# Performance work log

Measured on AMD Instinct MI355X. Metric: run time of the kernel, lower is better.

The kernel has to match this reference:

```python
import jax, jax.numpy as jnp
import numpy as np

B, S, D, H = 16, 1024, 512, 8
SCALES = (5, 10, None)


def setup_inputs() -> dict:
    key = jax.random.key(0)
    ks = jax.random.split(key, 7)
    x = jax.random.normal(ks[0], (B, S, D), jnp.float32)
    Wqkv = jax.random.normal(ks[1], (3, 3 * D, D), jnp.float32) * 0.02
    bqkv = jax.random.normal(ks[2], (3, 3 * D), jnp.float32) * 0.02
    Wo = jax.random.normal(ks[3], (3, D, D), jnp.float32) * 0.02
    bo = jax.random.normal(ks[4], (3, D), jnp.float32) * 0.02
    Wf = jax.random.normal(ks[5], (D, 3 * D), jnp.float32) * 0.02
    bf = jax.random.normal(ks[6], (D,), jnp.float32) * 0.02
    return {"x": x, "Wqkv": Wqkv, "bqkv": bqkv, "Wo": Wo, "bo": bo, "Wf": Wf, "bf": bf}


def _window_bias(seq_len, scale):
    # query j attends key k iff 0 <= j - k < scale (causal local window)
    i = jnp.arange(seq_len)
    d = i[:, None] - i[None, :]
    allowed = (d >= 0) & (d < scale)
    return jnp.where(allowed, 0.0, -jnp.inf).astype(jnp.float32)  # [S, S]


def _mha(x, Wqkv, bqkv, Wo, bo, bias):
    # x: [B, S, D]; packed in_proj like nn.MultiheadAttention
    b, s, d = x.shape
    hd = d // H
    qkv = x @ Wqkv.T + bqkv                      # [B, S, 3D]
    q, k, v = jnp.split(qkv, 3, axis=-1)
    q = q.reshape(b, s, H, hd) * (1.0 / np.sqrt(hd)).astype(x.dtype)
    k = k.reshape(b, s, H, hd)
    v = v.reshape(b, s, H, hd)
    scores = jnp.einsum("bqhd,bkhd->bhqk", q, k)  # [B, H, S, S]
    if bias is not None:
        scores = scores + bias                    # broadcast [S, S]
    p = jax.nn.softmax(scores, axis=-1)
    o = jnp.einsum("bhqk,bkhd->bqhd", p, v).reshape(b, s, d)
    return o @ Wo.T + bo


def reference(x, Wqkv, bqkv, Wo, bo, Wf, bf):
    s = x.shape[1]
    outs = []
    for i, scale in enumerate(SCALES):
        bias = None if scale is None else _window_bias(s, scale)
        outs.append(_mha(x, Wqkv[i], bqkv[i], Wo[i], bo[i], bias))
    combined = jnp.concatenate(outs, axis=-1)     # [B, S, 3D]
    return combined @ Wf.T + bf                   # [B, S, D]
```

## Files before the change

kernel.cpp:

```cpp
#include <hip/hip_runtime.h>
#include <hip/hip_bf16.h>
#include <hip/hip_fp16.h>


using f16 = _Float16;
typedef _Float16 f16x8 __attribute__((ext_vector_type(8)));
typedef _Float16 f16x2 __attribute__((ext_vector_type(2)));
typedef float    f32x4 __attribute__((ext_vector_type(4)));

__device__ inline void storeC(float* p, float v) { *p = v; }
__device__ inline void storeC(f16* p, float v)   { *p = (f16)v; }

__device__ inline void async_cp16(const f16* g, f16* l) {
    __builtin_amdgcn_global_load_lds(
        (const __attribute__((address_space(1))) unsigned int*)g,
        (__attribute__((address_space(3))) unsigned int*)l,
        16, 0, 0);
}

__global__ __launch_bounds__(256) void prep_all(
    const float* __restrict__ x, const float* __restrict__ Wqkv,
    const float* __restrict__ Wf, const float* __restrict__ Wo,
    const float* __restrict__ bo, const float* __restrict__ bfv,
    f16* __restrict__ xh, f16* __restrict__ wqkvh, f16* __restrict__ wfh,
    f16* __restrict__ WoT, float* __restrict__ bp)
{
    __shared__ float t[32][33];
    const int bid = blockIdx.x;
    const int tid = threadIdx.x;

    if (bid < 5632) {
        const float* in; f16* outp; int base;
        if (bid < 4096)      { in = x;    outp = xh;    base = bid; }
        else if (bid < 5248) { in = Wqkv; outp = wqkvh; base = bid - 4096; }
        else                 { in = Wf;   outp = wfh;   base = bid - 5248; }
        int i = (base * 256 + tid) * 8;
        float4 a = *(const float4*)(in + i);
        float4 b = *(const float4*)(in + i + 4);
        f16x8 h = { (f16)a.x, (f16)a.y, (f16)a.z, (f16)a.w,
                    (f16)b.x, (f16)b.y, (f16)b.z, (f16)b.w };
        *(f16x8*)(outp + i) = h;
    } else if (bid < 6400) {
        const int idx = bid - 5632;
        const int z  = idx >> 8;
        const int bx = (idx & 15) * 32;
        const int by = ((idx >> 4) & 15) * 32;
        const int tx = tid & 31;
        const int ty = tid >> 5;
#pragma unroll
        for (int r = ty; r < 32; r += 8)
            t[r][tx] = Wo[(size_t)z * 262144 + (by + r) * 512 + bx + tx];
        __syncthreads();
#pragma unroll
        for (int r = ty; r < 32; r += 8)
            WoT[(size_t)z * 262144 + (bx + r) * 512 + by + tx] = (f16)t[tx][r];
    } else {
        const int o = (bid - 6400) * 4 + (tid >> 6);
        const int lane = tid & 63;
        float s = 0.f;
        for (int j = lane; j < 1536; j += 64) s += Wf[o * 1536 + j] * bo[j];
#pragma unroll
        for (int msk = 1; msk < 64; msk <<= 1) s += __shfl_xor(s, msk, 64);
        if (lane == 0) bp[o] = s + bfv[o];
    }
}

template <typename TC>
__global__ __launch_bounds__(256) void gemm_mfma_nt(
    const f16* __restrict__ A, int lda, long azs,
    const f16* __restrict__ B, int ldb, long bzs,
    const float* __restrict__ bias,
    TC* __restrict__ C, int ldc, long czs,
    int K)
{
    __shared__ __align__(16) f16 As[2][128 * 32];
    __shared__ __align__(16) f16 Bs[2][128 * 32];

    const int tid  = threadIdx.x;
    const int lane = tid & 63;
    const int wave = tid >> 6;
    const int wm = (wave >> 1) * 64;
    const int wn = (wave & 1) * 64;
    const int bm = blockIdx.y * 128;
    const int bn = blockIdx.x * 128;
    const int z  = blockIdx.z;

    const int srow = tid >> 2;
    const int scol = (tid & 3) * 8;
    const int soff = srow * 32 + scol;

    const f16* Ag = A + (size_t)z * azs + (size_t)(bm + srow) * lda + scol;
    const f16* Bg = B + (size_t)z * bzs + (size_t)(bn + srow) * ldb + scol;

    f32x4 acc[4][4];
#pragma unroll
    for (int i = 0; i < 4; ++i)
#pragma unroll
        for (int j = 0; j < 4; ++j)
            acc[i][j] = (f32x4){0.f, 0.f, 0.f, 0.f};

    const int fr = lane & 15;
    const int fk = (lane >> 4) * 8;

    async_cp16(Ag, &As[0][soff]);
    async_cp16(Ag + (size_t)64 * lda, &As[0][soff + 64 * 32]);
    async_cp16(Bg, &Bs[0][soff]);
    async_cp16(Bg + (size_t)64 * ldb, &Bs[0][soff + 64 * 32]);

    const int nt = K >> 5;
    for (int t = 0; t < nt; ++t) {
        __syncthreads();
        const int p = t & 1;
        if (t + 1 < nt) {
            const int k1 = (t + 1) * 32;
            async_cp16(Ag + k1, &As[p ^ 1][soff]);
            async_cp16(Ag + k1 + (size_t)64 * lda, &As[p ^ 1][soff + 64 * 32]);
            async_cp16(Bg + k1, &Bs[p ^ 1][soff]);
            async_cp16(Bg + k1 + (size_t)64 * ldb, &Bs[p ^ 1][soff + 64 * 32]);
        }

        f16x8 af[4], bfr[4];
#pragma unroll
        for (int i = 0; i < 4; ++i)
            af[i] = *(const f16x8*)&As[p][(wm + i * 16 + fr) * 32 + fk];
#pragma unroll
        for (int j = 0; j < 4; ++j)
            bfr[j] = *(const f16x8*)&Bs[p][(wn + j * 16 + fr) * 32 + fk];
#pragma unroll
        for (int i = 0; i < 4; ++i)
#pragma unroll
            for (int j = 0; j < 4; ++j)
                acc[i][j] = __builtin_amdgcn_mfma_f32_16x16x32_f16(
                    af[i], bfr[j], acc[i][j], 0, 0, 0);
    }

    const int cn  = lane & 15;
    const int cr4 = (lane >> 4) * 4;
#pragma unroll
    for (int i = 0; i < 4; ++i) {
#pragma unroll
        for (int j = 0; j < 4; ++j) {
            const int col = bn + wn + j * 16 + cn;
            const float bv = bias ? bias[col] : 0.f;
#pragma unroll
            for (int r = 0; r < 4; ++r) {
                const int row = bm + wm + i * 16 + cr4 + r;
                storeC(&C[(size_t)z * czs + (size_t)row * ldc + col],
                       acc[i][j][r] + bv);
            }
        }
    }
}

template <int NR, typename TC>
__global__ __launch_bounds__(512, 2) void gemm_mfma_8ph(
    const f16* __restrict__ A, int lda,
    const f16* __restrict__ B, int ldb,
    const float* __restrict__ bias,
    TC* __restrict__ C, int ldc, int K)
{
    __shared__ __align__(16) f16 As[2][256 * 64];
    __shared__ __align__(16) f16 Bs[2][NR * 64 * 64];

    const int tid  = threadIdx.x;
    const int lane = tid & 63;
    const int wave = tid >> 6;
    const int wr = wave >> 2;
    const int wc = wave & 3;
    const int bm = blockIdx.y * 256;
    const int bn = blockIdx.x * (NR * 64);
    const int fr  = lane & 15;
    const int grp = lane >> 4;

    const int c0 = ((0 + grp) ^ (fr & 7)) * 8;
    const int c1 = ((4 + grp) ^ (fr & 7)) * 8;

    const int srow = tid >> 3;
    const int scol = ((tid & 7) ^ (srow & 7)) * 8;
    const f16* Ag = A + (size_t)(bm + srow) * lda + scol;
    const f16* Bg = B + (size_t)(bn + srow) * ldb + scol;

    f32x4 acc[8][NR];
#pragma unroll
    for (int m = 0; m < 8; ++m)
#pragma unroll
        for (int n = 0; n < NR; ++n)
            acc[m][n] = (f32x4){0.f, 0.f, 0.f, 0.f};

    const int arow = wr * 128 + fr;
    const int brow = wc * (NR * 16) + fr;

    f16x8 bfrag[NR][2];
    f16x8 aP[2][2], aQ[2][2];

    auto stage = [&](int p, int kt) {
        const f16* a_ = Ag + (size_t)kt * 64;
        const f16* b_ = Bg + (size_t)kt * 64;
        f16* al = &As[p][tid * 8];
        f16* bl = &Bs[p][tid * 8];
#pragma unroll
        for (int i = 0; i < 4; ++i)
            async_cp16(a_ + (size_t)(i * 64) * lda, al + i * 4096);
#pragma unroll
        for (int i = 0; i < NR; ++i)
            async_cp16(b_ + (size_t)(i * 64) * ldb, bl + i * 4096);
    };

    const int nt = K >> 6;

    stage(0, 0);
    stage(1, 1);

    for (int t = 0; t < nt; ++t) {
        const int p = t & 1;
        if (t + 1 < nt) {
            if constexpr (NR == 3)
                asm volatile("s_waitcnt vmcnt(7)" ::: "memory");
            else
                asm volatile("s_waitcnt vmcnt(6)" ::: "memory");
        } else {
            asm volatile("s_waitcnt vmcnt(0)" ::: "memory");
        }
        __builtin_amdgcn_s_barrier();

        const f16* asb = As[p];
        const f16* bsb = Bs[p];

        auto loada = [&](f16x8 (&d)[2][2], int mq) {
#pragma unroll
            for (int m2 = 0; m2 < 2; ++m2) {
                const int ro = (arow + (mq * 2 + m2) * 16) * 64;
                d[m2][0] = *(const f16x8*)&asb[ro + c0];
                d[m2][1] = *(const f16x8*)&asb[ro + c1];
            }
        };
        auto qmfma = [&](const f16x8 (&a_)[2][2], int mq) {
            __builtin_amdgcn_s_setprio(1);
#pragma unroll
            for (int m2 = 0; m2 < 2; ++m2)
#pragma unroll
                for (int n = 0; n < NR; ++n) {
                    f32x4 z = __builtin_amdgcn_mfma_f32_16x16x32_f16(
                        a_[m2][0], bfrag[n][0], acc[mq * 2 + m2][n], 0, 0, 0);
                    acc[mq * 2 + m2][n] = __builtin_amdgcn_mfma_f32_16x16x32_f16(
                        a_[m2][1], bfrag[n][1], z, 0, 0, 0);
                }
            __builtin_amdgcn_s_setprio(0);
        };

#pragma unroll
        for (int n = 0; n < NR; ++n) {
            const int ro = (brow + n * 16) * 64;
            bfrag[n][0] = *(const f16x8*)&bsb[ro + c0];
            bfrag[n][1] = *(const f16x8*)&bsb[ro + c1];
        }
        loada(aP, 0);
        asm volatile("s_waitcnt lgkmcnt(0)" ::: "memory");
        __builtin_amdgcn_sched_barrier(0);

        loada(aQ, 1);
        qmfma(aP, 0);
        asm volatile("s_waitcnt lgkmcnt(0)" ::: "memory");
        __builtin_amdgcn_sched_barrier(0);

        loada(aP, 2);
        qmfma(aQ, 1);
        asm volatile("s_waitcnt lgkmcnt(0)" ::: "memory");
        __builtin_amdgcn_sched_barrier(0);

        loada(aQ, 3);
        qmfma(aP, 2);
        asm volatile("s_waitcnt lgkmcnt(0)" ::: "memory");
        __builtin_amdgcn_sched_barrier(0);

        __builtin_amdgcn_s_barrier();
        if (t + 2 < nt) stage(p, t + 2);
        qmfma(aQ, 3);
    }

    const int cn  = lane & 15;
    const int cr4 = (lane >> 4) * 4;
#pragma unroll
    for (int m = 0; m < 8; ++m)
#pragma unroll
        for (int n = 0; n < NR; ++n) {
            const int col = bn + wc * (NR * 16) + n * 16 + cn;
            const float bv = bias ? bias[col] : 0.f;
#pragma unroll
            for (int r = 0; r < 4; ++r) {
                const int row = bm + wr * 128 + m * 16 + cr4 + r;
                storeC(&C[(size_t)row * ldc + col], acc[m][n][r] + bv);
            }
        }
}

__global__ __launch_bounds__(256) void win_attn_mfma(
    const f16* __restrict__ qkv, f16* __restrict__ out, int w)
{
    __shared__ __align__(16) f16 Vs[4][64 * 40];
    __shared__ __align__(16) f16 Ps[4][16 * 40];

    const int tid  = threadIdx.x;
    const int lane = tid & 63;
    const int wave = tid >> 6;
    const int b  = blockIdx.y;
    const int h  = blockIdx.z;
    const int q0 = (blockIdx.x * 4 + wave) * 16;
    const size_t bs = (size_t)b * 1024;

    const int fr  = lane & 15;
    const int grp = lane >> 4;
    const int fk8 = grp * 8;

    f16x8 aq[2];
    {
        const f16* qp = qkv + (bs + q0 + fr) * 1536 + h * 64 + fk8;
        aq[0] = *(const f16x8*)qp;
        aq[1] = *(const f16x8*)(qp + 32);
#pragma unroll
        for (int e = 0; e < 8; ++e) {
            aq[0][e] *= (f16)0.18033688;
            aq[1][e] *= (f16)0.18033688;
        }
    }

    f16x8 bk[2][2];
#pragma unroll
    for (int g = 0; g < 2; ++g) {
        int krow = q0 - 16 + g * 16 + fr;
        int kcl  = krow < 0 ? 0 : krow;
        const f16* kp = qkv + (bs + kcl) * 1536 + 512 + h * 64 + fk8;
        bk[g][0] = *(const f16x8*)kp;
        bk[g][1] = *(const f16x8*)(kp + 32);
    }

    {
        const int vk = lane & 31;
        const int vd = (lane >> 5) * 32;
        int vrow = q0 - 16 + vk;
        int vcl  = vrow < 0 ? 0 : vrow;
        const f16* vp = qkv + (bs + vcl) * 1536 + 1024 + h * 64 + vd;
        f16* vsw = Vs[wave];
#pragma unroll
        for (int t = 0; t < 4; ++t) {
            f16x8 vv = *(const f16x8*)(vp + t * 8);
#pragma unroll
            for (int e = 0; e < 8; ++e)
                vsw[(vd + t * 8 + e) * 40 + vk] = vv[e];
        }
    }

    f32x4 s[2];
#pragma unroll
    for (int g = 0; g < 2; ++g) {
        f32x4 z = (f32x4){0.f, 0.f, 0.f, 0.f};
        z = __builtin_amdgcn_mfma_f32_16x16x32_f16(aq[0], bk[g][0], z, 0, 0, 0);
        s[g] = __builtin_amdgcn_mfma_f32_16x16x32_f16(aq[1], bk[g][1], z, 0, 0, 0);
    }

    float l[4] = {0.f, 0.f, 0.f, 0.f};
#pragma unroll
    for (int g = 0; g < 2; ++g) {
        const int kpos = q0 - 16 + g * 16 + fr;
#pragma unroll
        for (int r = 0; r < 4; ++r) {
            const int diff = (grp * 4 + r) - (g * 16 + fr) + 16;
            const bool ok = (diff >= 0) && (diff < w) && (kpos >= 0);
            float p = ok ? exp2f(fminf(s[g][r], 15.9f)) : 0.f;
            l[r] += p;
            Ps[wave][(grp * 4 + r) * 40 + g * 16 + fr] = (f16)p;
        }
    }

    __builtin_amdgcn_wave_barrier();

    f16x8 pa = *(const f16x8*)&Ps[wave][fr * 40 + fk8];
    f32x4 acc[4];
#pragma unroll
    for (int j = 0; j < 4; ++j) {
        f16x8 bv = *(const f16x8*)&Vs[wave][(j * 16 + fr) * 40 + fk8];
        f32x4 z = (f32x4){0.f, 0.f, 0.f, 0.f};
        acc[j] = __builtin_amdgcn_mfma_f32_16x16x32_f16(pa, bv, z, 0, 0, 0);
    }

#pragma unroll
    for (int r = 0; r < 4; ++r)
#pragma unroll
        for (int msk = 1; msk < 16; msk <<= 1)
            l[r] += __shfl_xor(l[r], msk, 64);

#pragma unroll
    for (int j = 0; j < 4; ++j)
#pragma unroll
        for (int r = 0; r < 4; ++r) {
            const int q = q0 + grp * 4 + r;
            out[(bs + q) * 1536 + h * 64 + j * 16 + fr] = (f16)(acc[j][r] / l[r]);
        }
}

__global__ __launch_bounds__(256, 4) void full_attn_mfma(
    const f16* __restrict__ qkv, f16* __restrict__ out)
{
    __shared__ __align__(16) f16 Ks[2][64 * 72];
    __shared__ __align__(16) f16 Vs[2][64 * 72];

    const int tid  = threadIdx.x;
    const int lane = tid & 63;
    const int wave = tid >> 6;
    const int q0 = blockIdx.x * 128;
    const int b  = blockIdx.y;
    const int h  = blockIdx.z;
    const size_t bs = (size_t)b * 1024;

    const int fr  = lane & 15;
    const int grp = lane >> 4;
    const int fk8 = grp * 8;

    f16x8 aq[2][2];
#pragma unroll
    for (int qt = 0; qt < 2; ++qt) {
        const f16* qp = qkv + (bs + q0 + wave * 32 + qt * 16 + fr) * 1536
                        + h * 64 + fk8;
        aq[qt][0] = *(const f16x8*)qp;
        aq[qt][1] = *(const f16x8*)(qp + 32);
#pragma unroll
        for (int e = 0; e < 8; ++e) {
            aq[qt][0][e] *= (f16)0.18033688;
            aq[qt][1][e] *= (f16)0.18033688;
        }
    }

    f16x8 onesf;
#pragma unroll
    for (int e = 0; e < 8; ++e) onesf[e] = (f16)1.0f;

    const f32x4 fz = (f32x4){0.f, 0.f, 0.f, 0.f};
    f32x4 lacc[2] = {fz, fz};
    f32x4 acc[2][4];
#pragma unroll
    for (int qt = 0; qt < 2; ++qt)
#pragma unroll
        for (int j = 0; j < 4; ++j)
            acc[qt][j] = fz;

    const int kr = tid >> 2, kc = (tid & 3) * 16;
    const int kp = (tid & 31) * 2, cb = (tid >> 5) * 8;

    const f16* kgp = qkv + (bs + kr) * 1536 + 512 + h * 64 + kc;
    const f16* vgp = qkv + (bs + kp) * 1536 + 1024 + h * 64 + cb;

    f16x8 ka, kb, va, vb;
    ka = *(const f16x8*)kgp; kb = *(const f16x8*)(kgp + 8);
    va = *(const f16x8*)vgp; vb = *(const f16x8*)(vgp + 1536);

    {
        f16* ks = &Ks[0][kr * 72 + kc];
        *(f16x8*)ks = ka; *(f16x8*)(ks + 8) = kb;
        f16* vs = &Vs[0][kp];
#pragma unroll
        for (int e = 0; e < 8; ++e) {
            f16x2 pr = { va[e], vb[e] };
            *(f16x2*)&vs[(cb + e) * 72] = pr;
        }
    }
    kgp += 64 * 1536; vgp += 64 * 1536;
    ka = *(const f16x8*)kgp; kb = *(const f16x8*)(kgp + 8);
    va = *(const f16x8*)vgp; vb = *(const f16x8*)(vgp + 1536);

    for (int t = 0; t < 16; ++t) {
        __syncthreads();
        const int p = t & 1;

        if (t + 1 < 16) {
            f16* ks = &Ks[p ^ 1][kr * 72 + kc];
            *(f16x8*)ks = ka; *(f16x8*)(ks + 8) = kb;
            f16* vs = &Vs[p ^ 1][kp];
#pragma unroll
            for (int e = 0; e < 8; ++e) {
                f16x2 pr = { va[e], vb[e] };
                *(f16x2*)&vs[(cb + e) * 72] = pr;
            }
            if (t + 2 < 16) {
                kgp += 64 * 1536; vgp += 64 * 1536;
                ka = *(const f16x8*)kgp; kb = *(const f16x8*)(kgp + 8);
                va = *(const f16x8*)vgp; vb = *(const f16x8*)(vgp + 1536);
            }
        }

        f16x8 kf[4][2];
#pragma unroll
        for (int j = 0; j < 4; ++j)
#pragma unroll
            for (int c = 0; c < 2; ++c)
                kf[j][c] = *(const f16x8*)&Ks[p][(j * 16 + fr) * 72 + c * 32 + fk8];

        f16x8 paf[2][2];
#pragma unroll
        for (int qt = 0; qt < 2; ++qt) {
            f32x4 s2[4];
#pragma unroll
            for (int j = 0; j < 4; ++j) {
                f32x4 z = __builtin_amdgcn_mfma_f32_16x16x32_f16(
                        kf[j][0], aq[qt][0], fz, 0, 0, 0);
                s2[j] = __builtin_amdgcn_mfma_f32_16x16x32_f16(
                        kf[j][1], aq[qt][1], z, 0, 0, 0);
            }

            unsigned int dw[4][2];
#pragma unroll
            for (int j = 0; j < 4; ++j) {
                float p0 = exp2f(fminf(s2[j][0], 15.9f));
                float p1 = exp2f(fminf(s2[j][1], 15.9f));
                float p2 = exp2f(fminf(s2[j][2], 15.9f));
                float p3 = exp2f(fminf(s2[j][3], 15.9f));
                f16x2 h0 = { (f16)p0, (f16)p1 };
                f16x2 h1 = { (f16)p2, (f16)p3 };
                dw[j][0] = __builtin_bit_cast(unsigned int, h0);
                dw[j][1] = __builtin_bit_cast(unsigned int, h1);
            }

            unsigned int pdw[2][4];
#pragma unroll
            for (int c = 0; c < 2; ++c)
#pragma unroll
                for (int T = 0; T < 2; ++T) {
                    unsigned int X = dw[2 * c][T];
                    unsigned int Y = dw[2 * c + 1][T];
                    asm("v_permlane32_swap_b32 %0, %1" : "+v"(X), "+v"(Y));
                    asm("v_permlane16_swap_b32 %0, %1" : "+v"(X), "+v"(Y));
                    pdw[c][T]     = X;
                    pdw[c][2 + T] = Y;
                }
            union { unsigned int u[4]; f16x8 hv; } cu;
#pragma unroll
            for (int c = 0; c < 2; ++c) {
                cu.u[0] = pdw[c][0]; cu.u[1] = pdw[c][1];
                cu.u[2] = pdw[c][2]; cu.u[3] = pdw[c][3];
                paf[qt][c] = cu.hv;
            }

            lacc[qt] = __builtin_amdgcn_mfma_f32_16x16x32_f16(
                paf[qt][0], onesf, lacc[qt], 0, 0, 0);
            lacc[qt] = __builtin_amdgcn_mfma_f32_16x16x32_f16(
                paf[qt][1], onesf, lacc[qt], 0, 0, 0);
        }

        f16x8 vf[4][2];
#pragma unroll
        for (int j = 0; j < 4; ++j)
#pragma unroll
            for (int c = 0; c < 2; ++c)
                vf[j][c] = *(const f16x8*)&Vs[p][(j * 16 + fr) * 72 + c * 32 + fk8];

#pragma unroll
        for (int qt = 0; qt < 2; ++qt)
#pragma unroll
            for (int j = 0; j < 4; ++j)
#pragma unroll
                for (int c = 0; c < 2; ++c)
                    acc[qt][j] = __builtin_amdgcn_mfma_f32_16x16x32_f16(
                        paf[qt][c], vf[j][c], acc[qt][j], 0, 0, 0);
    }

#pragma unroll
    for (int qt = 0; qt < 2; ++qt) {
        float inv[4];
#pragma unroll
        for (int r = 0; r < 4; ++r) inv[r] = 1.0f / lacc[qt][r];
#pragma unroll
        for (int j = 0; j < 4; ++j)
#pragma unroll
            for (int r = 0; r < 4; ++r) {
                const int q = q0 + wave * 32 + qt * 16 + grp * 4 + r;
                out[(bs + q) * 1536 + h * 64 + j * 16 + fr] =
                    (f16)(acc[qt][j][r] * inv[r]);
            }
    }
}

extern "C" void kernel_launch(void* const* d_in, const int* in_sizes, int n_in,
                              void* d_out, int out_size, void* d_ws, size_t ws_size,
                              hipStream_t stream)
{
    const float* x    = (const float*)d_in[0];
    const float* Wqkv = (const float*)d_in[1];
    const float* bqkv = (const float*)d_in[2];
    const float* Wo   = (const float*)d_in[3];
    const float* bo   = (const float*)d_in[4];
    const float* Wf   = (const float*)d_in[5];
    const float* bfin = (const float*)d_in[6];
    float* out = (float*)d_out;

    char* ws = (char*)d_ws;
    f16*   qkvbuf   = (f16*)ws;
    f16*   attn_cat = (f16*)(ws + 50331648);
    f16*   wfh      = (f16*)(ws + 100663296);
    f16*   WoT      = (f16*)(ws + 102236160);
    f16*   Wfo      = (f16*)(ws + 103809024);
    float* bp       = (float*)(ws + 105381888);

    f16* xh    = (f16*)d_out;
    f16* wqkvh = (f16*)((char*)d_out + 16777216);

    prep_all<<<dim3(6528), 256, 0, stream>>>(
        x, Wqkv, Wf, Wo, bo, bfin, xh, wqkvh, wfh, WoT, bp);

    gemm_mfma_nt<f16><<<dim3(4, 4, 3), 256, 0, stream>>>(
        wfh, 1536, 512, WoT, 512, 262144, nullptr, Wfo, 1536, 512, 512);

    for (int i = 0; i < 3; ++i) {
        gemm_mfma_8ph<3, f16><<<dim3(8, 64), 512, 0, stream>>>(
            xh, 512, wqkvh + (size_t)i * 786432, 512, bqkv + i * 1536,
            qkvbuf, 1536, 512);

        if (i == 0)
            win_attn_mfma<<<dim3(16, 16, 8), 256, 0, stream>>>(
                qkvbuf, attn_cat + 0 * 512, 5);
        else if (i == 1)
            win_attn_mfma<<<dim3(16, 16, 8), 256, 0, stream>>>(
                qkvbuf, attn_cat + 1 * 512, 10);
        else
            full_attn_mfma<<<dim3(8, 16, 8), 256, 0, stream>>>(
                qkvbuf, attn_cat + 2 * 512);
    }

    gemm_mfma_8ph<2, float><<<dim3(4, 64), 512, 0, stream>>>(
        attn_cat, 1536, Wfo, 1536, bp, out, 512, 1536);
}
```

Baseline: 386.4 us.

## Batch the three QKV GEMMs and fuse all attention branches into one launch

The three per-scale QKV projections become a single batched GEMM launch using blockIdx.z strides, and each scale writes to its own QKV buffer. All three attention variants then run in one combined kernel that dispatches on block index, with the full-attention blocks scheduled first. The windowed attention body also keeps P in registers through permlane swaps and computes row sums with an MFMA against ones, instead of staging P in LDS and reducing with shuffles. The aim is fewer launches and tail gaps plus better occupancy overlap, at the cost of three times the QKV workspace, which is taken only if ws_size is large enough.

```diff
diff --git a/kernel.cpp b/kernel.cpp
--- a/kernel.cpp
+++ b/kernel.cpp
@@ -155,12 +155,17 @@
 template <int NR, typename TC>
 __global__ __launch_bounds__(512, 2) void gemm_mfma_8ph(
     const f16* __restrict__ A, int lda,
-    const f16* __restrict__ B, int ldb,
-    const float* __restrict__ bias,
-    TC* __restrict__ C, int ldc, int K)
+    const f16* __restrict__ B, int ldb, long bzs,
+    const float* __restrict__ bias, long bizs,
+    TC* __restrict__ C, int ldc, long czs, int K)
 {
     __shared__ __align__(16) f16 As[2][256 * 64];
     __shared__ __align__(16) f16 Bs[2][NR * 64 * 64];
+
+    const int z = blockIdx.z;
+    B += (size_t)z * bzs;
+    C += (size_t)z * czs;
+    const float* biasz = bias ? bias + (size_t)z * bizs : nullptr;
 
     const int tid  = threadIdx.x;
     const int lane = tid & 63;
@@ -207,7 +212,6 @@
     };
 
     const int nt = K >> 6;
-
     stage(0, 0);
     stage(1, 1);
 
@@ -240,10 +244,10 @@
             for (int m2 = 0; m2 < 2; ++m2)
 #pragma unroll
                 for (int n = 0; n < NR; ++n) {
-                    f32x4 z = __builtin_amdgcn_mfma_f32_16x16x32_f16(
+                    f32x4 zz = __builtin_amdgcn_mfma_f32_16x16x32_f16(
                         a_[m2][0], bfrag[n][0], acc[mq * 2 + m2][n], 0, 0, 0);
                     acc[mq * 2 + m2][n] = __builtin_amdgcn_mfma_f32_16x16x32_f16(
-                        a_[m2][1], bfrag[n][1], z, 0, 0, 0);
+                        a_[m2][1], bfrag[n][1], zz, 0, 0, 0);
                 }
             __builtin_amdgcn_s_setprio(0);
         };
@@ -285,7 +289,7 @@
 #pragma unroll
         for (int n = 0; n < NR; ++n) {
             const int col = bn + wc * (NR * 16) + n * 16 + cn;
-            const float bv = bias ? bias[col] : 0.f;
+            const float bv = biasz ? biasz[col] : 0.f;
 #pragma unroll
             for (int r = 0; r < 4; ++r) {
                 const int row = bm + wr * 128 + m * 16 + cr4 + r;
@@ -294,23 +298,21 @@
         }
 }
 
-__global__ __launch_bounds__(256) void win_attn_mfma(
-    const f16* __restrict__ qkv, f16* __restrict__ out, int w)
-{
-    __shared__ __align__(16) f16 Vs[4][64 * 40];
-    __shared__ __align__(16) f16 Ps[4][16 * 40];
-
+__device__ __forceinline__ void win_attn_body(
+    const f16* __restrict__ qkv, f16* __restrict__ out, f16* sm,
+    int w, int bx, int b, int h)
+{
     const int tid  = threadIdx.x;
     const int lane = tid & 63;
     const int wave = tid >> 6;
-    const int b  = blockIdx.y;
-    const int h  = blockIdx.z;
-    const int q0 = (blockIdx.x * 4 + wave) * 16;
+    const int q0 = (bx * 4 + wave) * 16;
     const size_t bs = (size_t)b * 1024;
 
     const int fr  = lane & 15;
     const int grp = lane >> 4;
     const int fk8 = grp * 8;
+
+    f16* vsw = sm + wave * 2560;
 
     f16x8 aq[2];
     {
@@ -340,7 +342,6 @@
         int vrow = q0 - 16 + vk;
         int vcl  = vrow < 0 ? 0 : vrow;
         const f16* vp = qkv + (bs + vcl) * 1536 + 1024 + h * 64 + vd;
-        f16* vsw = Vs[wave];
 #pragma unroll
         for (int t = 0; t < 4; ++t) {
             f16x8 vv = *(const f16x8*)(vp + t * 8);
@@ -350,66 +351,83 @@
         }
     }
 
+    const f32x4 fz = (f32x4){0.f, 0.f, 0.f, 0.f};
     f32x4 s[2];
 #pragma unroll
     for (int g = 0; g < 2; ++g) {
-        f32x4 z = (f32x4){0.f, 0.f, 0.f, 0.f};
-        z = __builtin_amdgcn_mfma_f32_16x16x32_f16(aq[0], bk[g][0], z, 0, 0, 0);
-        s[g] = __builtin_amdgcn_mfma_f32_16x16x32_f16(aq[1], bk[g][1], z, 0, 0, 0);
-    }
-
-    float l[4] = {0.f, 0.f, 0.f, 0.f};
+        f32x4 z = __builtin_amdgcn_mfma_f32_16x16x32_f16(
+            bk[g][0], aq[0], fz, 0, 0, 0);
+        s[g] = __builtin_amdgcn_mfma_f32_16x16x32_f16(
+            bk[g][1], aq[1], z, 0, 0, 0);
+    }
+
+    unsigned int dw[2][2];
 #pragma unroll
     for (int g = 0; g < 2; ++g) {
-        const int kpos = q0 - 16 + g * 16 + fr;
+        float p[4];
 #pragma unroll
         for (int r = 0; r < 4; ++r) {
-            const int diff = (grp * 4 + r) - (g * 16 + fr) + 16;
+            const int kin  = g * 16 + grp * 4 + r;
+            const int kpos = q0 - 16 + kin;
+            const int diff = fr - kin + 16;
             const bool ok = (diff >= 0) && (diff < w) && (kpos >= 0);
-            float p = ok ? exp2f(fminf(s[g][r], 15.9f)) : 0.f;
-            l[r] += p;
-            Ps[wave][(grp * 4 + r) * 40 + g * 16 + fr] = (f16)p;
-        }
-    }
+            p[r] = ok ? exp2f(fminf(s[g][r], 15.9f)) : 0.f;
+        }
+        f16x2 h0 = { (f16)p[0], (f16)p[1] };
+        f16x2 h1 = { (f16)p[2], (f16)p[3] };
+        dw[g][0] = __builtin_bit_cast(unsigned int, h0);
+        dw[g][1] = __builtin_bit_cast(unsigned int, h1);
+    }
+
+    unsigned int pdw[4];
+#pragma unroll
+    for (int T = 0; T < 2; ++T) {
+        unsigned int X = dw[0][T];
+        unsigned int Y = dw[1][T];
+        asm("v_permlane32_swap_b32 %0, %1" : "+v"(X), "+v"(Y));
+        asm("v_permlane16_swap_b32 %0, %1" : "+v"(X), "+v"(Y));
+        pdw[T]     = X;
+        pdw[2 + T] = Y;
+    }
+    union { unsigned int u[4]; f16x8 hv; } cu;
+    cu.u[0] = pdw[0]; cu.u[1] = pdw[1]; cu.u[2] = pdw[2]; cu.u[3] = pdw[3];
+    const f16x8 paf = cu.hv;
+
+    f16x8 onesf;
+#pragma unroll
+    for (int e = 0; e < 8; ++e) onesf[e] = (f16)1.0f;
+    f32x4 lacc = __builtin_amdgcn_mfma_f32_16x16x32_f16(paf, onesf, fz, 0, 0, 0);
 
     __builtin_amdgcn_wave_barrier();
 
-    f16x8 pa = *(const f16x8*)&Ps[wave][fr * 40 + fk8];
     f32x4 acc[4];
 #pragma unroll
     for (int j = 0; j < 4; ++j) {
-        f16x8 bv = *(const f16x8*)&Vs[wave][(j * 16 + fr) * 40 + fk8];
-        f32x4 z = (f32x4){0.f, 0.f, 0.f, 0.f};
-        acc[j] = __builtin_amdgcn_mfma_f32_16x16x32_f16(pa, bv, z, 0, 0, 0);
-    }
-
-#pragma unroll
-    for (int r = 0; r < 4; ++r)
-#pragma unroll
-        for (int msk = 1; msk < 16; msk <<= 1)
-            l[r] += __shfl_xor(l[r], msk, 64);
-
+        f16x8 bv = *(const f16x8*)&vsw[(j * 16 + fr) * 40 + fk8];
+        acc[j] = __builtin_amdgcn_mfma_f32_16x16x32_f16(paf, bv, fz, 0, 0, 0);
+    }
+
+    float inv[4];
+#pragma unroll
+    for (int r = 0; r < 4; ++r) inv[r] = 1.0f / lacc[r];
 #pragma unroll
     for (int j = 0; j < 4; ++j)
 #pragma unroll
         for (int r = 0; r < 4; ++r) {
             const int q = q0 + grp * 4 + r;
-            out[(bs + q) * 1536 + h * 64 + j * 16 + fr] = (f16)(acc[j][r] / l[r]);
-        }
-}
-
-__global__ __launch_bounds__(256, 4) void full_attn_mfma(
-    const f16* __restrict__ qkv, f16* __restrict__ out)
-{
-    __shared__ __align__(16) f16 Ks[2][64 * 72];
-    __shared__ __align__(16) f16 Vs[2][64 * 72];
-
+            out[(bs + q) * 1536 + h * 64 + j * 16 + fr] =
+                (f16)(acc[j][r] * inv[r]);
+        }
+}
+
+__device__ __forceinline__ void full_attn_body(
+    const f16* __restrict__ qkv, f16* __restrict__ out, f16* sm,
+    int bx, int b, int h)
+{
     const int tid  = threadIdx.x;
     const int lane = tid & 63;
     const int wave = tid >> 6;
-    const int q0 = blockIdx.x * 128;
-    const int b  = blockIdx.y;
-    const int h  = blockIdx.z;
+    const int q0 = bx * 128;
     const size_t bs = (size_t)b * 1024;
 
     const int fr  = lane & 15;
@@ -454,9 +472,9 @@
     va = *(const f16x8*)vgp; vb = *(const f16x8*)(vgp + 1536);
 
     {
-        f16* ks = &Ks[0][kr * 72 + kc];
+        f16* ks = sm + kr * 72 + kc;
         *(f16x8*)ks = ka; *(f16x8*)(ks + 8) = kb;
-        f16* vs = &Vs[0][kp];
+        f16* vs = sm + 9216 + kp;
 #pragma unroll
         for (int e = 0; e < 8; ++e) {
             f16x2 pr = { va[e], vb[e] };
@@ -470,11 +488,13 @@
     for (int t = 0; t < 16; ++t) {
         __syncthreads();
         const int p = t & 1;
+        const f16* Ksp = sm + p * 4608;
+        const f16* Vsp = sm + 9216 + p * 4608;
 
         if (t + 1 < 16) {
-            f16* ks = &Ks[p ^ 1][kr * 72 + kc];
+            f16* ks = sm + (p ^ 1) * 4608 + kr * 72 + kc;
             *(f16x8*)ks = ka; *(f16x8*)(ks + 8) = kb;
-            f16* vs = &Vs[p ^ 1][kp];
+            f16* vs = sm + 9216 + (p ^ 1) * 4608 + kp;
 #pragma unroll
             for (int e = 0; e < 8; ++e) {
                 f16x2 pr = { va[e], vb[e] };
@@ -492,7 +512,7 @@
         for (int j = 0; j < 4; ++j)
 #pragma unroll
             for (int c = 0; c < 2; ++c)
-                kf[j][c] = *(const f16x8*)&Ks[p][(j * 16 + fr) * 72 + c * 32 + fk8];
+                kf[j][c] = *(const f16x8*)&Ksp[(j * 16 + fr) * 72 + c * 32 + fk8];
 
         f16x8 paf[2][2];
 #pragma unroll
@@ -550,7 +570,7 @@
         for (int j = 0; j < 4; ++j)
 #pragma unroll
             for (int c = 0; c < 2; ++c)
-                vf[j][c] = *(const f16x8*)&Vs[p][(j * 16 + fr) * 72 + c * 32 + fk8];
+                vf[j][c] = *(const f16x8*)&Vsp[(j * 16 + fr) * 72 + c * 32 + fk8];
 
 #pragma unroll
         for (int qt = 0; qt < 2; ++qt)
@@ -575,6 +595,37 @@
                 out[(bs + q) * 1536 + h * 64 + j * 16 + fr] =
                     (f16)(acc[qt][j][r] * inv[r]);
             }
+    }
+}
+
+__global__ __launch_bounds__(256) void win_attn_mfma(
+    const f16* __restrict__ qkv, f16* __restrict__ out, int w)
+{
+    __shared__ __align__(16) f16 sm[4 * 2560];
+    win_attn_body(qkv, out, sm, w, blockIdx.x, blockIdx.y, blockIdx.z);
+}
+
+__global__ __launch_bounds__(256, 4) void full_attn_mfma(
+    const f16* __restrict__ qkv, f16* __restrict__ out)
+{
+    __shared__ __align__(16) f16 sm[18432];
+    full_attn_body(qkv, out, sm, blockIdx.x, blockIdx.y, blockIdx.z);
+}
+
+__global__ __launch_bounds__(256, 4) void attn_all(
+    const f16* __restrict__ q0b, const f16* __restrict__ q1b,
+    const f16* __restrict__ q2b, f16* __restrict__ cat)
+{
+    __shared__ __align__(16) f16 sm[18432];
+    const int bid = blockIdx.x;
+    if (bid < 1024) {
+        full_attn_body(q2b, cat + 1024, sm, bid & 7, (bid >> 3) & 15, bid >> 7);
+    } else if (bid < 3072) {
+        const int i = bid - 1024;
+        win_attn_body(q0b, cat, sm, 5, i & 15, (i >> 4) & 15, i >> 8);
+    } else {
+        const int i = bid - 3072;
+        win_attn_body(q1b, cat + 512, sm, 10, i & 15, (i >> 4) & 15, i >> 8);
     }
 }
 
@@ -591,39 +642,69 @@
     const float* bfin = (const float*)d_in[6];
     float* out = (float*)d_out;
 
-    char* ws = (char*)d_ws;
-    f16*   qkvbuf   = (f16*)ws;
-    f16*   attn_cat = (f16*)(ws + 50331648);
-    f16*   wfh      = (f16*)(ws + 100663296);
-    f16*   WoT      = (f16*)(ws + 102236160);
-    f16*   Wfo      = (f16*)(ws + 103809024);
-    float* bp       = (float*)(ws + 105381888);
-
     f16* xh    = (f16*)d_out;
     f16* wqkvh = (f16*)((char*)d_out + 16777216);
-
-    prep_all<<<dim3(6528), 256, 0, stream>>>(
-        x, Wqkv, Wf, Wo, bo, bfin, xh, wqkvh, wfh, WoT, bp);
-
-    gemm_mfma_nt<f16><<<dim3(4, 4, 3), 256, 0, stream>>>(
-        wfh, 1536, 512, WoT, 512, 262144, nullptr, Wfo, 1536, 512, 512);
-
-    for (int i = 0; i < 3; ++i) {
-        gemm_mfma_8ph<3, f16><<<dim3(8, 64), 512, 0, stream>>>(
-            xh, 512, wqkvh + (size_t)i * 786432, 512, bqkv + i * 1536,
-            qkvbuf, 1536, 512);
-
-        if (i == 0)
-            win_attn_mfma<<<dim3(16, 16, 8), 256, 0, stream>>>(
-                qkvbuf, attn_cat + 0 * 512, 5);
-        else if (i == 1)
-            win_attn_mfma<<<dim3(16, 16, 8), 256, 0, stream>>>(
-                qkvbuf, attn_cat + 1 * 512, 10);
-        else
-            full_attn_mfma<<<dim3(8, 16, 8), 256, 0, stream>>>(
-                qkvbuf, attn_cat + 2 * 512);
-    }
-
-    gemm_mfma_8ph<2, float><<<dim3(4, 64), 512, 0, stream>>>(
-        attn_cat, 1536, Wfo, 1536, bp, out, 512, 1536);
-}
+    char* ws = (char*)d_ws;
+
+    const size_t QKV_EL = 25165824;
+    const size_t QKV_B  = 50331648;
+
+    const bool fused = ws_size >= (size_t)206047232;
+
+    if (fused) {
+        f16*   qkv0     = (f16*)ws;
+        f16*   attn_cat = (f16*)(ws + 3 * QKV_B);
+        f16*   wfh      = (f16*)(ws + 3 * QKV_B + QKV_B);
+        f16*   WoT      = (f16*)((char*)wfh + 1572864);
+        f16*   Wfo      = (f16*)((char*)WoT + 1572864);
+        float* bp       = (float*)((char*)Wfo + 1572864);
+
+        prep_all<<<dim3(6528), 256, 0, stream>>>(
+            x, Wqkv, Wf, Wo, bo, bfin, xh, wqkvh, wfh, WoT, bp);
+
+        gemm_mfma_nt<f16><<<dim3(4, 4, 3), 256, 0, stream>>>(
+            wfh, 1536, 512, WoT, 512, 262144, nullptr, Wfo, 1536, 512, 512);
+
+        gemm_mfma_8ph<3, f16><<<dim3(8, 64, 3), 512, 0, stream>>>(
+            xh, 512, wqkvh, 512, 786432, bqkv, 1536,
+            qkv0, 1536, (long)QKV_EL, 512);
+
+        attn_all<<<dim3(5120), 256, 0, stream>>>(
+            qkv0, qkv0 + QKV_EL, qkv0 + 2 * QKV_EL, attn_cat);
+
+        gemm_mfma_8ph<2, float><<<dim3(4, 64, 1), 512, 0, stream>>>(
+            attn_cat, 1536, Wfo, 1536, 0, bp, 0, out, 512, 0, 1536);
+    } else {
+        f16*   qkvbuf   = (f16*)ws;
+        f16*   attn_cat = (f16*)(ws + QKV_B);
+        f16*   wfh      = (f16*)(ws + 2 * QKV_B);
+        f16*   WoT      = (f16*)(ws + 2 * QKV_B + 1572864);
+        f16*   Wfo      = (f16*)(ws + 2 * QKV_B + 2 * 1572864);
+        float* bp       = (float*)(ws + 2 * QKV_B + 3 * 1572864);
+
+        prep_all<<<dim3(6528), 256, 0, stream>>>(
+            x, Wqkv, Wf, Wo, bo, bfin, xh, wqkvh, wfh, WoT, bp);
+
+        gemm_mfma_nt<f16><<<dim3(4, 4, 3), 256, 0, stream>>>(
+            wfh, 1536, 512, WoT, 512, 262144, nullptr, Wfo, 1536, 512, 512);
+
+        for (int i = 0; i < 3; ++i) {
+            gemm_mfma_8ph<3, f16><<<dim3(8, 64, 1), 512, 0, stream>>>(
+                xh, 512, wqkvh + (size_t)i * 786432, 512, 0,
+                bqkv + i * 1536, 0, qkvbuf, 1536, 0, 512);
+
+            if (i == 0)
+                win_attn_mfma<<<dim3(16, 16, 8), 256, 0, stream>>>(
+                    qkvbuf, attn_cat + 0 * 512, 5);
+            else if (i == 1)
+                win_attn_mfma<<<dim3(16, 16, 8), 256, 0, stream>>>(
+                    qkvbuf, attn_cat + 1 * 512, 10);
+            else
+                full_attn_mfma<<<dim3(8, 16, 8), 256, 0, stream>>>(
+                    qkvbuf, attn_cat + 2 * 512);
+        }
+
+        gemm_mfma_8ph<2, float><<<dim3(4, 64, 1), 512, 0, stream>>>(
+            attn_cat, 1536, Wfo, 1536, 0, bp, 0, out, 512, 0, 1536);
+    }
+}
```

Result: faster. 369.6 us (-4.3%).
